# Optimization experiments

Measured on AMD Instinct MI355X. Metric: run time of the kernel, lower is better.

Reference implementation:

```python
import jax, jax.numpy as jnp
import numpy as np

MC = 64  # mc_samples; fill=1.0 -> k == k_ball so neighbor ordering is irrelevant


def swish(x):
    return x * jax.nn.sigmoid(x)


def setup_inputs() -> dict:
    key = jax.random.key(0)
    ks = jax.random.split(key, 12)
    bs, n, g_dim = 4, 1024, 6
    c_in = c_out = 256
    H, hid = 8, 16

    def lin(k, i, o):
        return (jax.random.normal(k, (i, o), jnp.float32) / np.sqrt(i).astype(np.float32))

    return {
        "pairwise_g": jax.random.normal(ks[0], (bs, n, n, g_dim), jnp.float32),
        "coset_functions": jax.random.normal(ks[1], (bs, n, c_in), jnp.float32),
        "mask": jax.random.randint(ks[2], (bs, n), 0, 2) > 0,
        # per-head location-kernel MLP (MultiheadWeightNet: g_dim -> hid -> hid -> 1)
        "loc_W1": jax.random.normal(ks[3], (H, g_dim, hid), jnp.float32) / np.sqrt(g_dim).astype(np.float32),
        "loc_b1": jnp.zeros((H, hid), jnp.float32),
        "loc_W2": jax.random.normal(ks[4], (H, hid, hid), jnp.float32) / np.sqrt(hid).astype(np.float32),
        "loc_b2": jnp.zeros((H, hid), jnp.float32),
        "loc_W3": jax.random.normal(ks[5], (H, hid, 1), jnp.float32) / np.sqrt(hid).astype(np.float32),
        "loc_b3": jnp.zeros((H, 1), jnp.float32),
        # DotProductKernel projections
        "Wq": lin(ks[6], c_in, c_in), "bq": jnp.zeros((c_in,), jnp.float32),
        "Wk": lin(ks[7], c_in, c_in), "bk": jnp.zeros((c_in,), jnp.float32),
        # value (input_linear) and output projections
        "W_in": lin(ks[8], c_in, c_out), "b_in": jnp.zeros((c_out,), jnp.float32),
        "W_out": lin(ks[9], c_out, c_out), "b_out": jnp.zeros((c_out,), jnp.float32),
    }


def reference(pairwise_g, coset_functions, mask, loc_W1, loc_b1, loc_W2, loc_b2,
              loc_W3, loc_b3, Wq, bq, Wk, bk, W_in, b_in, W_out, b_out):
    bs, n, _, g_dim = pairwise_g.shape
    c_in = coset_functions.shape[-1]
    H = loc_W1.shape[0]
    dh = c_in // H
    b_idx = jnp.arange(bs)[:, None, None]

    # --- neighbourhood extraction: topk (smallest) group distances, masked keys pushed far away
    dists = jnp.linalg.norm(pairwise_g, axis=-1)                  # (b,n,n)
    dists = jnp.where(mask[:, None, :], dists, jnp.float32(1e8))
    _, nbhd_idx = jax.lax.top_k(-dists, MC)                       # (b,n,m) nearest MC keys
    nbhd_g = jnp.take_along_axis(pairwise_g, nbhd_idx[..., None], axis=2)  # (b,n,m,g)
    nbhd_mask = mask[b_idx, nbhd_idx]                             # (b,n,m)

    # --- location kernel: per-head MLP on gathered pairwise group elements
    h = swish(jnp.einsum('bnmg,hgk->bnmhk', nbhd_g, loc_W1) + loc_b1)
    h = swish(jnp.einsum('bnmhk,hkl->bnmhl', h, loc_W2) + loc_b2)
    loc = swish(jnp.einsum('bnmhk,hko->bnmho', h, loc_W3) + loc_b3)[..., 0]  # (b,n,m,H)

    # --- feature kernel: dot-product scores on gathered keys
    q = (coset_functions @ Wq + bq).reshape(bs, n, H, dh)
    k = (coset_functions @ Wk + bk).reshape(bs, n, H, dh)
    k_nbhd = k[b_idx, nbhd_idx]                                   # (b,n,m,H,dh)
    feat = jnp.einsum('bnhd,bnmhd->bnmh', q, k_nbhd) / np.sqrt(dh).astype(np.float32)

    # --- masked softmax over the neighbourhood dim (dim 2)
    scores = jnp.where(nbhd_mask[..., None], loc + feat, jnp.float32(-1e38))
    attn = jax.nn.softmax(scores, axis=2)                         # (b,n,m,H)

    # --- value projection + sparse attention (equivalent to the dense scatter+matmul,
    #     since topk neighbour indices are unique per query)
    v = (coset_functions @ W_in + b_in).reshape(bs, n, H, dh)
    v_nbhd = v[b_idx, nbhd_idx]                                   # (b,n,m,H,dh)
    out = jnp.einsum('bnmh,bnmhd->bnhd', attn, v_nbhd).reshape(bs, n, H * dh)
    out = out @ W_out + b_out
    return (pairwise_g, out, mask)
```

## Files before the change

kernel.cpp:

```cpp
#include <hip/hip_runtime.h>
#include <stdint.h>

#define BS 4
#define NN 1024
#define GD 6
#define CIN 256
#define NH 8
#define DH 32
#define HID 16
#define MCS 64

#define PG_ELEMS (BS*NN*NN*GD)
#define OUT_OFF  PG_ELEMS
#define MASK_OFF (PG_ELEMS + BS*NN*CIN)

typedef float vfloat4 __attribute__((ext_vector_type(4)));

__device__ __forceinline__ float swishf(float x) {
    return x * (1.0f / (1.0f + __expf(-x)));
}

__global__ __launch_bounds__(256) void gemm3(const float* __restrict__ X,
    const float* __restrict__ W0, const float* __restrict__ B0, float* __restrict__ D0,
    const float* __restrict__ W1, const float* __restrict__ B1, float* __restrict__ D1,
    const float* __restrict__ W2, const float* __restrict__ B2, float* __restrict__ D2)
{
    const float* W; const float* Bv; float* D;
    if (blockIdx.y == 0)      { W = W0; Bv = B0; D = D0; }
    else if (blockIdx.y == 1) { W = W1; Bv = B1; D = D1; }
    else                      { W = W2; Bv = B2; D = D2; }
    const int c  = threadIdx.x;
    const int r0 = blockIdx.x * 16;
    __shared__ float xs[16][CIN];
    #pragma unroll
    for (int r = 0; r < 16; ++r) xs[r][c] = X[(size_t)(r0 + r)*CIN + c];
    __syncthreads();
    float acc[16];
    #pragma unroll
    for (int r = 0; r < 16; ++r) acc[r] = 0.f;
    #pragma unroll 4
    for (int k = 0; k < CIN; ++k) {
        float w = W[(size_t)k*CIN + c];
        #pragma unroll
        for (int r = 0; r < 16; ++r) acc[r] += xs[r][k] * w;
    }
    float bb = Bv[c];
    #pragma unroll
    for (int r = 0; r < 16; ++r) D[(size_t)(r0 + r)*CIN + c] = acc[r] + bb;
}

__global__ __launch_bounds__(256, 7) void attn_topk(
    const float* __restrict__ pg, const int* __restrict__ mask,
    const float* __restrict__ lW1g, const float* __restrict__ lb1g,
    const float* __restrict__ lW2g, const float* __restrict__ lb2g,
    const float* __restrict__ lW3g, const float* __restrict__ lb3g,
    const float* __restrict__ Q, const float* __restrict__ Kc, const float* __restrict__ Vc,
    float* __restrict__ O, float* __restrict__ pg_out)
{
    const int i = blockIdx.x, b = blockIdx.y, tid = threadIdx.x;
    const int lane = tid & 63;

    __shared__ __align__(16) unsigned selbuf[512];
    __shared__ float sg[MCS*7];
    __shared__ int nj[MCS];
    __shared__ unsigned wsum[4];
    __shared__ unsigned sel_bin, sel_need, s_cnt, s_eqcnt;

    float (*sc)[NH]   = (float (*)[NH])selbuf;
    unsigned* hist    = selbuf;
    unsigned* eqlist  = selbuf + 256;

    const size_t rowoff = (size_t)(b*NN + i) * (NN*GD);
    const vfloat4* src4 = (const vfloat4*)(pg + rowoff);
    vfloat4* dst4 = (vfloat4*)(pg_out + rowoff);
    #pragma unroll
    for (int t = 0; t < 6; ++t) {
        vfloat4 v = src4[tid + 256*t];
        __builtin_nontemporal_store(v, &dst4[tid + 256*t]);
    }
    float qv = Q[(size_t)(b*NN + i)*CIN + tid];

    const int* mrow = mask + b*NN;
    const int4 mv = ((const int4*)mrow)[tid];
    const vfloat4* gg = src4 + tid*6;
    vfloat4 a0 = gg[0], a1 = gg[1], a2 = gg[2], a3 = gg[3], a4 = gg[4], a5 = gg[5];
    float rv[4][6];
    rv[0][0]=a0.x; rv[0][1]=a0.y; rv[0][2]=a0.z; rv[0][3]=a0.w; rv[0][4]=a1.x; rv[0][5]=a1.y;
    rv[1][0]=a1.z; rv[1][1]=a1.w; rv[1][2]=a2.x; rv[1][3]=a2.y; rv[1][4]=a2.z; rv[1][5]=a2.w;
    rv[2][0]=a3.x; rv[2][1]=a3.y; rv[2][2]=a3.z; rv[2][3]=a3.w; rv[2][4]=a4.x; rv[2][5]=a4.y;
    rv[3][0]=a4.z; rv[3][1]=a4.w; rv[3][2]=a5.x; rv[3][3]=a5.y; rv[3][4]=a5.z; rv[3][5]=a5.w;
    const int vb[4] = { mv.x, mv.y, mv.z, mv.w };
    unsigned key[4];
    #pragma unroll
    for (int r = 0; r < 4; ++r) {
        float d2 = rv[r][0]*rv[r][0] + rv[r][1]*rv[r][1] + rv[r][2]*rv[r][2]
                 + rv[r][3]*rv[r][3] + rv[r][4]*rv[r][4] + rv[r][5]*rv[r][5];
        key[r] = __float_as_uint(vb[r] ? d2 : 1e30f);
    }

    unsigned prefix = 0;
    int need = MCS;
    for (int level = 0; level < 4; ++level) {
        const int shift = 24 - 8*level;
        hist[tid] = 0;
        __syncthreads();
        if (level == 0) {
            #pragma unroll
            for (int r = 0; r < 4; ++r) {
                unsigned d = key[r] >> 24;
                unsigned long long todo = __ballot(true);
                while (todo) {
                    int leader = (int)(__ffsll((unsigned long long)todo) - 1);
                    unsigned dl = __shfl(d, leader);
                    unsigned long long match = __ballot(d == dl);
                    if (lane == leader) atomicAdd(&hist[dl], (unsigned)__popcll(match));
                    todo &= ~match;
                }
            }
        } else {
            const unsigned pmask = 0xFFFFFFFFu << (shift + 8);
            #pragma unroll
            for (int r = 0; r < 4; ++r)
                if ((key[r] & pmask) == prefix)
                    atomicAdd(&hist[(key[r] >> shift) & 0xFFu], 1u);
        }
        __syncthreads();
        unsigned own = hist[tid];
        unsigned v = own;
        #pragma unroll
        for (int off = 1; off < 64; off <<= 1) {
            unsigned nv = __shfl_up(v, off);
            if (lane >= off) v += nv;
        }
        if (lane == 63) wsum[tid >> 6] = v;
        __syncthreads();
        unsigned basec = 0;
        for (int w = 0; w < (tid >> 6); ++w) basec += wsum[w];
        unsigned incl = v + basec;
        unsigned excl = incl - own;
        if (excl < (unsigned)need && (unsigned)need <= incl) {
            sel_bin = (unsigned)tid;
            sel_need = (unsigned)need - excl;
        }
        __syncthreads();
        prefix |= (sel_bin << shift);
        need = (int)sel_need;
    }
    const unsigned T = prefix;
    const int needT = need;

    if (tid == 0) { s_cnt = 0; s_eqcnt = 0; }
    __syncthreads();
    #pragma unroll
    for (int r = 0; r < 4; ++r) {
        unsigned kk = key[r];
        int j = tid*4 + r;
        if (kk < T) {
            unsigned p = atomicAdd(&s_cnt, 1u);
            nj[p] = j | (vb[r] ? 0 : (int)0x80000000);
            #pragma unroll
            for (int g = 0; g < GD; ++g) sg[p*7 + g] = rv[r][g];
        } else if (kk == T) {
            unsigned e = atomicAdd(&s_eqcnt, 1u);
            if (e < 64) eqlist[e] = (unsigned)j;
        }
    }
    __syncthreads();
    const int cbase = (int)s_cnt;
    if (tid == 0) {
        int ec = (int)s_eqcnt; if (ec > 64) ec = 64;
        for (int s2 = 0; s2 < needT; ++s2) {
            int bi = -1, bj = 0x7FFFFFFF;
            for (int e = 0; e < ec; ++e) {
                int jj = (int)eqlist[e];
                if (jj < bj) { bj = jj; bi = e; }
            }
            if (bi >= 0) {
                eqlist[bi] = 0x7FFFFFFFu;
                nj[cbase + s2] = bj | (mrow[bj] ? 0 : (int)0x80000000);
            }
        }
    }
    __syncthreads();
    #pragma unroll
    for (int r = 0; r < 4; ++r) {
        if (key[r] == T) {
            int j = tid*4 + r;
            for (int s2 = 0; s2 < needT; ++s2)
                if ((nj[cbase + s2] & 0x7FFFFFFF) == j) {
                    #pragma unroll
                    for (int g = 0; g < GD; ++g) sg[(cbase + s2)*7 + g] = rv[r][g];
                }
        }
    }
    __syncthreads();

    #pragma unroll
    for (int pass = 0; pass < 2; ++pass) {
        const int h = __builtin_amdgcn_readfirstlane((tid >> 6) + pass*4);
        const int m = lane;
        const float* W1h = lW1g + h*(GD*HID);
        const float* B1h = lb1g + h*HID;
        const float* W2h = lW2g + h*(HID*HID);
        const float* B2h = lb2g + h*HID;
        const float* W3h = lW3g + h*HID;
        float gv[GD];
        #pragma unroll
        for (int g = 0; g < GD; ++g) gv[g] = sg[m*7 + g];
        float h1[HID];
        #pragma unroll
        for (int kk = 0; kk < HID; ++kk) {
            float a = B1h[kk];
            #pragma unroll
            for (int g = 0; g < GD; ++g) a += gv[g] * W1h[g*HID + kk];
            h1[kk] = swishf(a);
        }
        float h2[HID];
        #pragma unroll
        for (int l = 0; l < HID; ++l) {
            float a = B2h[l];
            #pragma unroll
            for (int kk = 0; kk < HID; ++kk) a += h1[kk] * W2h[kk*HID + l];
            h2[l] = swishf(a);
        }
        float a3 = lb3g[h];
        #pragma unroll
        for (int kk = 0; kk < HID; ++kk) a3 += h2[kk] * W3h[kk];
        sc[m][h] = swishf(a3);
    }
    __syncthreads();

    {
        const float scale = 0.17677669529663688f;
        const int hh = tid >> 5;
        #pragma unroll 4
        for (int m = 0; m < MCS; ++m) {
            int code = nj[m];
            int jm = code & 0x7FFFFFFF;
            float kv = Kc[(size_t)(b*NN + jm)*CIN + tid] * qv;
            kv += __shfl_xor(kv, 16);
            kv += __shfl_xor(kv, 8);
            kv += __shfl_xor(kv, 4);
            kv += __shfl_xor(kv, 2);
            kv += __shfl_xor(kv, 1);
            if ((tid & 31) == 0) {
                float s = sc[m][hh] + kv * scale;
                if (code < 0) s = -1e38f;
                sc[m][hh] = s;
            }
        }
    }
    __syncthreads();

    #pragma unroll
    for (int pass = 0; pass < 2; ++pass) {
        int h = (tid >> 6) + pass*4;
        float s = sc[lane][h];
        float mx = s;
        #pragma unroll
        for (int off = 32; off; off >>= 1) mx = fmaxf(mx, __shfl_xor(mx, off));
        float e = __expf(s - mx);
        float sum = e;
        #pragma unroll
        for (int off = 32; off; off >>= 1) sum += __shfl_xor(sum, off);
        sc[lane][h] = e / sum;
    }
    __syncthreads();

    {
        const int hh = tid >> 5;
        float acc = 0.f;
        #pragma unroll 8
        for (int m = 0; m < MCS; ++m) {
            int jm = nj[m] & 0x7FFFFFFF;
            acc += sc[m][hh] * Vc[(size_t)(b*NN + jm)*CIN + tid];
        }
        O[(size_t)(b*NN + i)*CIN + tid] = acc;
    }
}

__global__ __launch_bounds__(256) void write_mask(const int* __restrict__ mask, float* __restrict__ dst) {
    int t = blockIdx.x*256 + threadIdx.x;
    if (t < BS*NN) dst[t] = mask[t] ? 1.0f : 0.0f;
}

extern "C" void kernel_launch(void* const* d_in, const int* in_sizes, int n_in,
                              void* d_out, int out_size, void* d_ws, size_t ws_size,
                              hipStream_t stream) {
    const float* pg   = (const float*)d_in[0];
    const float* x    = (const float*)d_in[1];
    const int*   mask = (const int*)d_in[2];
    const float* lW1  = (const float*)d_in[3];
    const float* lb1  = (const float*)d_in[4];
    const float* lW2  = (const float*)d_in[5];
    const float* lb2  = (const float*)d_in[6];
    const float* lW3  = (const float*)d_in[7];
    const float* lb3  = (const float*)d_in[8];
    const float* Wq   = (const float*)d_in[9];
    const float* bq   = (const float*)d_in[10];
    const float* Wk   = (const float*)d_in[11];
    const float* bk   = (const float*)d_in[12];
    const float* Wv   = (const float*)d_in[13];
    const float* bv   = (const float*)d_in[14];
    const float* Wo   = (const float*)d_in[15];
    const float* bo   = (const float*)d_in[16];

    float* out = (float*)d_out;
    float* Q  = (float*)d_ws;
    float* Kc = Q  + (size_t)BS*NN*CIN;
    float* Vc = Kc + (size_t)BS*NN*CIN;
    float* O  = Vc + (size_t)BS*NN*CIN;

    gemm3<<<dim3(BS*NN/16, 3), 256, 0, stream>>>(x, Wq, bq, Q, Wk, bk, Kc, Wv, bv, Vc);
    attn_topk<<<dim3(NN, BS), 256, 0, stream>>>(pg, mask, lW1, lb1, lW2, lb2, lW3, lb3,
                                                Q, Kc, Vc, O, out);
    gemm3<<<dim3(BS*NN/16, 1), 256, 0, stream>>>(O, Wo, bo, out + OUT_OFF,
                                                 Wo, bo, out + OUT_OFF,
                                                 Wo, bo, out + OUT_OFF);
    write_mask<<<dim3(16), 256, 0, stream>>>(mask, out + MASK_OFF);
}
```

Baseline: 387.5 us.

## Vectorize gathers and GEMM, fold mask write into attention kernel, fast math

The projection GEMM now computes a 4x4 register tile per thread, reading float4 weight vectors against a transposed shared-memory copy of the input rows. In the attention kernel, the key and value gathers load float4 per thread over a split of the neighbour set, using precomputed row offsets; the partial value sums are reduced through shared memory. Swish and softmax use hardware exp2 and reciprocal intrinsics. The separate mask-writing kernel is merged into the attention kernel, and the occupancy hint rises to 8 blocks. Together these aim to cut gather latency, per-element load instructions and one launch, at the cost of approximate transcendentals and added shared-memory traffic.

```diff
diff --git a/kernel.cpp b/kernel.cpp
--- a/kernel.cpp
+++ b/kernel.cpp
@@ -15,9 +15,22 @@
 #define MASK_OFF (PG_ELEMS + BS*NN*CIN)
 
 typedef float vfloat4 __attribute__((ext_vector_type(4)));
+typedef unsigned vuint4 __attribute__((ext_vector_type(4)));
+
+#if __has_builtin(__builtin_amdgcn_rcpf)
+__device__ __forceinline__ float fast_rcp(float x) { return __builtin_amdgcn_rcpf(x); }
+#else
+__device__ __forceinline__ float fast_rcp(float x) { return 1.0f / x; }
+#endif
+#if __has_builtin(__builtin_amdgcn_exp2f)
+__device__ __forceinline__ float fast_exp2(float x) { return __builtin_amdgcn_exp2f(x); }
+#else
+__device__ __forceinline__ float fast_exp2(float x) { return exp2f(x); }
+#endif
+#define LOG2E 1.44269504088896340736f
 
 __device__ __forceinline__ float swishf(float x) {
-    return x * (1.0f / (1.0f + __expf(-x)));
+    return x * fast_rcp(1.0f + fast_exp2(x * -LOG2E));
 }
 
 __global__ __launch_bounds__(256) void gemm3(const float* __restrict__ X,
@@ -29,33 +42,51 @@
     if (blockIdx.y == 0)      { W = W0; Bv = B0; D = D0; }
     else if (blockIdx.y == 1) { W = W1; Bv = B1; D = D1; }
     else                      { W = W2; Bv = B2; D = D2; }
-    const int c  = threadIdx.x;
-    const int r0 = blockIdx.x * 16;
-    __shared__ float xs[16][CIN];
-    #pragma unroll
-    for (int r = 0; r < 16; ++r) xs[r][c] = X[(size_t)(r0 + r)*CIN + c];
-    __syncthreads();
-    float acc[16];
-    #pragma unroll
-    for (int r = 0; r < 16; ++r) acc[r] = 0.f;
+    const int tid = threadIdx.x;
+    const int c4  = tid & 63;
+    const int rg  = tid >> 6;
+    const int r0  = blockIdx.x * 16;
+
+    __shared__ float xsT[CIN][20];
+    {
+        float tmp[16];
+        #pragma unroll
+        for (int r = 0; r < 16; ++r) tmp[r] = X[(size_t)(r0 + r)*CIN + tid];
+        vfloat4* dst = (vfloat4*)&xsT[tid][0];
+        #pragma unroll
+        for (int j = 0; j < 4; ++j)
+            dst[j] = (vfloat4){tmp[4*j+0], tmp[4*j+1], tmp[4*j+2], tmp[4*j+3]};
+    }
+    __syncthreads();
+
+    vfloat4 a0 = (vfloat4){0.f,0.f,0.f,0.f};
+    vfloat4 a1 = a0, a2 = a0, a3 = a0;
+    const vfloat4* W4 = (const vfloat4*)W;
     #pragma unroll 4
     for (int k = 0; k < CIN; ++k) {
-        float w = W[(size_t)k*CIN + c];
-        #pragma unroll
-        for (int r = 0; r < 16; ++r) acc[r] += xs[r][k] * w;
-    }
-    float bb = Bv[c];
-    #pragma unroll
-    for (int r = 0; r < 16; ++r) D[(size_t)(r0 + r)*CIN + c] = acc[r] + bb;
+        vfloat4 w  = W4[(size_t)k*64 + c4];
+        vfloat4 xr = *(const vfloat4*)&xsT[k][rg*4];
+        a0 += xr.x * w;
+        a1 += xr.y * w;
+        a2 += xr.z * w;
+        a3 += xr.w * w;
+    }
+    vfloat4 bb = ((const vfloat4*)Bv)[c4];
+    vfloat4* D4 = (vfloat4*)D;
+    const size_t rbase = (size_t)(r0 + rg*4);
+    D4[(rbase+0)*64 + c4] = a0 + bb;
+    D4[(rbase+1)*64 + c4] = a1 + bb;
+    D4[(rbase+2)*64 + c4] = a2 + bb;
+    D4[(rbase+3)*64 + c4] = a3 + bb;
 }
 
-__global__ __launch_bounds__(256, 7) void attn_topk(
+__global__ __launch_bounds__(256, 8) void attn_topk(
     const float* __restrict__ pg, const int* __restrict__ mask,
     const float* __restrict__ lW1g, const float* __restrict__ lb1g,
     const float* __restrict__ lW2g, const float* __restrict__ lb2g,
     const float* __restrict__ lW3g, const float* __restrict__ lb3g,
     const float* __restrict__ Q, const float* __restrict__ Kc, const float* __restrict__ Vc,
-    float* __restrict__ O, float* __restrict__ pg_out)
+    float* __restrict__ O, float* __restrict__ pg_out, float* __restrict__ mask_out)
 {
     const int i = blockIdx.x, b = blockIdx.y, tid = threadIdx.x;
     const int lane = tid & 63;
@@ -63,6 +94,8 @@
     __shared__ __align__(16) unsigned selbuf[512];
     __shared__ float sg[MCS*7];
     __shared__ int nj[MCS];
+    __shared__ __align__(16) unsigned joff[MCS];
+    __shared__ vfloat4 obuf[4][64];
     __shared__ unsigned wsum[4];
     __shared__ unsigned sel_bin, sel_need, s_cnt, s_eqcnt;
 
@@ -70,6 +103,9 @@
     unsigned* hist    = selbuf;
     unsigned* eqlist  = selbuf + 256;
 
+    const int* mrow = mask + b*NN;
+    if (tid == 0) mask_out[b*NN + i] = mrow[i] ? 1.0f : 0.0f;
+
     const size_t rowoff = (size_t)(b*NN + i) * (NN*GD);
     const vfloat4* src4 = (const vfloat4*)(pg + rowoff);
     vfloat4* dst4 = (vfloat4*)(pg_out + rowoff);
@@ -78,17 +114,16 @@
         vfloat4 v = src4[tid + 256*t];
         __builtin_nontemporal_store(v, &dst4[tid + 256*t]);
     }
-    float qv = Q[(size_t)(b*NN + i)*CIN + tid];
-
-    const int* mrow = mask + b*NN;
+    vfloat4 q4 = ((const vfloat4*)Q)[(size_t)(b*NN + i)*64 + (tid & 63)];
+
     const int4 mv = ((const int4*)mrow)[tid];
     const vfloat4* gg = src4 + tid*6;
-    vfloat4 a0 = gg[0], a1 = gg[1], a2 = gg[2], a3 = gg[3], a4 = gg[4], a5 = gg[5];
+    vfloat4 g0 = gg[0], g1 = gg[1], g2 = gg[2], g3 = gg[3], g4 = gg[4], g5 = gg[5];
     float rv[4][6];
-    rv[0][0]=a0.x; rv[0][1]=a0.y; rv[0][2]=a0.z; rv[0][3]=a0.w; rv[0][4]=a1.x; rv[0][5]=a1.y;
-    rv[1][0]=a1.z; rv[1][1]=a1.w; rv[1][2]=a2.x; rv[1][3]=a2.y; rv[1][4]=a2.z; rv[1][5]=a2.w;
-    rv[2][0]=a3.x; rv[2][1]=a3.y; rv[2][2]=a3.z; rv[2][3]=a3.w; rv[2][4]=a4.x; rv[2][5]=a4.y;
-    rv[3][0]=a4.z; rv[3][1]=a4.w; rv[3][2]=a5.x; rv[3][3]=a5.y; rv[3][4]=a5.z; rv[3][5]=a5.w;
+    rv[0][0]=g0.x; rv[0][1]=g0.y; rv[0][2]=g0.z; rv[0][3]=g0.w; rv[0][4]=g1.x; rv[0][5]=g1.y;
+    rv[1][0]=g1.z; rv[1][1]=g1.w; rv[1][2]=g2.x; rv[1][3]=g2.y; rv[1][4]=g2.z; rv[1][5]=g2.w;
+    rv[2][0]=g3.x; rv[2][1]=g3.y; rv[2][2]=g3.z; rv[2][3]=g3.w; rv[2][4]=g4.x; rv[2][5]=g4.y;
+    rv[3][0]=g4.z; rv[3][1]=g4.w; rv[3][2]=g5.x; rv[3][3]=g5.y; rv[3][4]=g5.z; rv[3][5]=g5.w;
     const int vb[4] = { mv.x, mv.y, mv.z, mv.w };
     unsigned key[4];
     #pragma unroll
@@ -195,6 +230,8 @@
     }
     __syncthreads();
 
+    if (tid < MCS) joff[tid] = ((unsigned)(b*NN + (nj[tid] & 0x7FFFFFFF))) << 6;
+
     #pragma unroll
     for (int pass = 0; pass < 2; ++pass) {
         const int h = __builtin_amdgcn_readfirstlane((tid >> 6) + pass*4);
@@ -226,28 +263,31 @@
         float a3 = lb3g[h];
         #pragma unroll
         for (int kk = 0; kk < HID; ++kk) a3 += h2[kk] * W3h[kk];
-        sc[m][h] = swishf(a3);
-    }
-    __syncthreads();
-
-    {
-        const float scale = 0.17677669529663688f;
-        const int hh = tid >> 5;
-        #pragma unroll 4
-        for (int m = 0; m < MCS; ++m) {
-            int code = nj[m];
-            int jm = code & 0x7FFFFFFF;
-            float kv = Kc[(size_t)(b*NN + jm)*CIN + tid] * qv;
-            kv += __shfl_xor(kv, 16);
-            kv += __shfl_xor(kv, 8);
-            kv += __shfl_xor(kv, 4);
-            kv += __shfl_xor(kv, 2);
-            kv += __shfl_xor(kv, 1);
-            if ((tid & 31) == 0) {
-                float s = sc[m][hh] + kv * scale;
-                if (code < 0) s = -1e38f;
-                sc[m][hh] = s;
-            }
+        sc[m][h] = (nj[m] < 0) ? -1e38f : swishf(a3);
+    }
+    __syncthreads();
+
+    const int q = tid & 63;
+    const int p = tid >> 6;
+    const int hh = q >> 3;
+    q4 *= 0.17677669529663688f;
+    const vfloat4* Kc4 = (const vfloat4*)Kc;
+    const vuint4* jo4 = (const vuint4*)(joff + (p << 4));
+    #pragma unroll
+    for (int mg = 0; mg < 4; ++mg) {
+        vuint4 o4 = jo4[mg];
+        #pragma unroll
+        for (int r = 0; r < 4; ++r) {
+            const int mm = (p << 4) + (mg << 2) + r;
+            vfloat4 kv = Kc4[o4[r] + (unsigned)q];
+            float d = q4.x * kv.x;
+            d = fmaf(q4.y, kv.y, d);
+            d = fmaf(q4.z, kv.z, d);
+            d = fmaf(q4.w, kv.w, d);
+            d += __shfl_xor(d, 1);
+            d += __shfl_xor(d, 2);
+            d += __shfl_xor(d, 4);
+            if ((q & 7) == 0) sc[mm][hh] += d;
         }
     }
     __syncthreads();
@@ -259,29 +299,36 @@
         float mx = s;
         #pragma unroll
         for (int off = 32; off; off >>= 1) mx = fmaxf(mx, __shfl_xor(mx, off));
-        float e = __expf(s - mx);
+        float e = fast_exp2((s - mx) * LOG2E);
         float sum = e;
         #pragma unroll
         for (int off = 32; off; off >>= 1) sum += __shfl_xor(sum, off);
-        sc[lane][h] = e / sum;
+        sc[lane][h] = e * fast_rcp(sum);
     }
     __syncthreads();
 
     {
-        const int hh = tid >> 5;
-        float acc = 0.f;
-        #pragma unroll 8
-        for (int m = 0; m < MCS; ++m) {
-            int jm = nj[m] & 0x7FFFFFFF;
-            acc += sc[m][hh] * Vc[(size_t)(b*NN + jm)*CIN + tid];
-        }
-        O[(size_t)(b*NN + i)*CIN + tid] = acc;
-    }
-}
-
-__global__ __launch_bounds__(256) void write_mask(const int* __restrict__ mask, float* __restrict__ dst) {
-    int t = blockIdx.x*256 + threadIdx.x;
-    if (t < BS*NN) dst[t] = mask[t] ? 1.0f : 0.0f;
+        const vfloat4* Vc4 = (const vfloat4*)Vc;
+        vfloat4 acc = (vfloat4){0.f,0.f,0.f,0.f};
+        #pragma unroll
+        for (int mg = 0; mg < 4; ++mg) {
+            vuint4 o4 = jo4[mg];
+            #pragma unroll
+            for (int r = 0; r < 4; ++r) {
+                const int mm = (p << 4) + (mg << 2) + r;
+                float a = sc[mm][hh];
+                vfloat4 v4 = Vc4[o4[r] + (unsigned)q];
+                acc += a * v4;
+            }
+        }
+        obuf[p][q] = acc;
+    }
+    __syncthreads();
+    {
+        const float* ob = (const float*)obuf;
+        float s = ob[tid] + ob[256 + tid] + ob[512 + tid] + ob[768 + tid];
+        O[(size_t)(b*NN + i)*CIN + tid] = s;
+    }
 }
 
 extern "C" void kernel_launch(void* const* d_in, const int* in_sizes, int n_in,
@@ -313,9 +360,8 @@
 
     gemm3<<<dim3(BS*NN/16, 3), 256, 0, stream>>>(x, Wq, bq, Q, Wk, bk, Kc, Wv, bv, Vc);
     attn_topk<<<dim3(NN, BS), 256, 0, stream>>>(pg, mask, lW1, lb1, lW2, lb2, lW3, lb3,
-                                                Q, Kc, Vc, O, out);
+                                                Q, Kc, Vc, O, out, out + MASK_OFF);
     gemm3<<<dim3(BS*NN/16, 1), 256, 0, stream>>>(O, Wo, bo, out + OUT_OFF,
                                                  Wo, bo, out + OUT_OFF,
                                                  Wo, bo, out + OUT_OFF);
-    write_mask<<<dim3(16), 256, 0, stream>>>(mask, out + MASK_OFF);
 }
```

Result: faster. 338.8 us (-12.6%).
